# Performance work log

Hardware: AMD Instinct MI355X
Metric: run time of the kernel (lower is better)

Reference implementation:

```python
import jax, jax.numpy as jnp
import numpy as np

THRESHOLD = 1.0  # snntorch Leaky default threshold
BETA = 0.9
ATAN_ALPHA = 2.0  # snntorch surrogate.atan default alpha

# Heaviside forward with ATan surrogate gradient (snntorch surrogate.atan)
@jax.custom_vjp
def atan_spike(x):
    return (x > 0).astype(x.dtype)

def _atan_fwd(x):
    return atan_spike(x), x

def _atan_bwd(x, g):
    # d/dx ~ (alpha/2) / (1 + (pi/2 * alpha * x)^2)
    return (g * (ATAN_ALPHA / 2.0) / (1.0 + (jnp.pi / 2.0 * ATAN_ALPHA * x) ** 2),)

atan_spike.defvjp(_atan_fwd, _atan_bwd)


def setup_inputs() -> dict:
    key = jax.random.key(0)
    kx, kw = jax.random.split(key)
    T, B, N_in, N_out = 128, 64, 1024, 1024
    x = (jax.random.uniform(kx, (T, B, N_in)) < 0.2).astype(jnp.float32)
    # kaiming_uniform_(mode='fan_in', nonlinearity='tanh'): gain=5/3, bound=gain*sqrt(3/fan_in)
    bound = (5.0 / 3.0) * np.sqrt(3.0 / N_in)
    W = jax.random.uniform(kw, (N_out, N_in), minval=-bound, maxval=bound, dtype=jnp.float32)
    return {"x": x, "W": W}


def reference(x, W):
    # x: (T, B, N_in) -> current: (T, B, N_out) via bias-free linear (vmapped over T)
    cur = jnp.einsum('tbi,oi->tbo', x, W)
    mem0 = jnp.zeros(cur.shape[1:], cur.dtype)

    # snntorch Leaky (reset_mechanism='subtract'):
    #   reset_t = detached spike of previous mem; mem_t = beta*mem_{t-1} + I_t - reset_t*thr
    #   spk_t = fire(mem_t)
    def step(mem, c_t):
        reset = jax.lax.stop_gradient(atan_spike(mem - THRESHOLD))
        mem_new = BETA * mem + c_t - reset * THRESHOLD
        spk = atan_spike(mem_new - THRESHOLD)
        return mem_new, (spk, mem_new)

    _, (spk_rec, mem_rec) = jax.lax.scan(step, mem0, cur)
    return spk_rec, mem_rec
```

## Files before the change

kernel.cpp:

```cpp
#include <hip/hip_runtime.h>
#include <cstddef>

constexpr int T_STEPS = 128;
constexpr int BATCH   = 64;
constexpr int N_IN    = 1024;
constexpr int N_OUT   = 1024;
constexpr int M_TOTAL = T_STEPS * BATCH;
constexpr int NEURONS = BATCH * N_OUT;
constexpr int OUT_HALF = T_STEPS * NEURONS;

constexpr double W_SCALE     = 17179869184.0;
constexpr double W_INV_SCALE = 1.0 / 17179869184.0;

typedef int   i32x4 __attribute__((ext_vector_type(4)));
typedef float f32x4 __attribute__((ext_vector_type(4)));

__global__ __launch_bounds__(256)
void prep_all(const float* __restrict__ x, const float* __restrict__ W,
              signed char* __restrict__ xi8, signed char* __restrict__ pi8)
{
    const int bid = blockIdx.x;
    if (bid < 2048) {
        const int i = bid * 256 + threadIdx.x;
        const float4 a = ((const float4*)x)[4 * i + 0];
        const float4 b = ((const float4*)x)[4 * i + 1];
        const float4 c = ((const float4*)x)[4 * i + 2];
        const float4 d = ((const float4*)x)[4 * i + 3];
        const float f[16] = {a.x,a.y,a.z,a.w, b.x,b.y,b.z,b.w,
                             c.x,c.y,c.z,c.w, d.x,d.y,d.z,d.w};
        union { signed char b[16]; int4 v; } u;
#pragma unroll
        for (int j = 0; j < 16; ++j) u.b[j] = (signed char)(f[j] != 0.0f);
        ((int4*)xi8)[i] = u.v;
    } else {
        const int i = (bid - 2048) * 256 + threadIdx.x;
        const float4 wv = ((const float4*)W)[i];
        const float wf[4] = {wv.x, wv.y, wv.z, wv.w};
        union { signed char b[4]; unsigned u; } dig[4];
#pragma unroll
        for (int j = 0; j < 4; ++j) {
            int q = __double2int_rn((double)wf[j] * W_SCALE);
            const int d0 = ((q + 128) & 255) - 128;  q = (q - d0) >> 8;
            const int d1 = ((q + 128) & 255) - 128;  q = (q - d1) >> 8;
            const int d2 = ((q + 128) & 255) - 128;  q = (q - d2) >> 8;
            dig[0].b[j] = (signed char)d0;
            dig[1].b[j] = (signed char)d1;
            dig[2].b[j] = (signed char)d2;
            dig[3].b[j] = (signed char)q;
        }
        unsigned* pw = (unsigned*)pi8;
#pragma unroll
        for (int p = 0; p < 4; ++p) pw[p * 262144 + i] = dig[p].u;
    }
}

constexpr int LDT = 80;

__global__ __launch_bounds__(512)
void gemm_planes(const signed char* __restrict__ xi8, const signed char* __restrict__ pi8,
                 unsigned* __restrict__ outw)
{
    __shared__ __align__(16) signed char As[128][LDT];
    __shared__ __align__(16) signed char Bs[4][128][LDT];

    const int tid  = threadIdx.x;
    const int m0   = blockIdx.x * 128;
    const int n0   = blockIdx.y * 128;
    const int lane = tid & 63;
    const int w    = tid >> 6;
    const int wm   = w >> 2;
    const int wn   = w & 3;
    const int l15  = lane & 15;
    const int kg   = lane >> 4;

    i32x4 acc[4][4][2] = {};

    const int arow = tid >> 2;
    const int aq   = tid & 3;

    for (int k0 = 0; k0 < N_IN; k0 += 64) {
        {
            const int4 v = *(const int4*)(xi8 + (size_t)(m0 + arow) * N_IN + k0 + aq * 16);
            *(int4*)(&As[arow][aq * 16]) = v;
        }
#pragma unroll
        for (int r = 0; r < 4; ++r) {
            const int u2  = tid + 512 * r;
            const int p   = u2 >> 9;
            const int rem = u2 & 511;
            const int row = rem >> 2;
            const int qq  = rem & 3;
            const int4 v = *(const int4*)(pi8 + (size_t)p * 1048576
                                              + (size_t)(n0 + row) * N_IN + k0 + qq * 16);
            *(int4*)(&Bs[p][row][qq * 16]) = v;
        }
        __syncthreads();

        i32x4 af[4], bf[2][4];
#pragma unroll
        for (int fm = 0; fm < 4; ++fm)
            af[fm] = *(const i32x4*)(&As[wm * 64 + fm * 16 + l15][kg * 16]);
#pragma unroll
        for (int fn = 0; fn < 2; ++fn)
#pragma unroll
            for (int p = 0; p < 4; ++p)
                bf[fn][p] = *(const i32x4*)(&Bs[p][wn * 32 + fn * 16 + l15][kg * 16]);

#pragma unroll
        for (int p = 0; p < 4; ++p)
#pragma unroll
            for (int fm = 0; fm < 4; ++fm)
#pragma unroll
                for (int fn = 0; fn < 2; ++fn)
                    acc[p][fm][fn] = __builtin_amdgcn_mfma_i32_16x16x64_i8(
                        af[fm], bf[fn][p], acc[p][fm][fn], 0, 0, 0);
        __syncthreads();
    }

#pragma unroll
    for (int fm = 0; fm < 4; ++fm)
#pragma unroll
        for (int fn = 0; fn < 2; ++fn)
#pragma unroll
            for (int r = 0; r < 4; ++r) {
                const int m = m0 + wm * 64 + fm * 16 + kg * 4 + r;
                const int o = n0 + wn * 32 + fn * 16 + l15;
                const double q = (double)acc[3][fm][fn][r] * 16777216.0
                               + (double)acc[2][fm][fn][r] * 65536.0
                               + (double)acc[1][fm][fn][r] * 256.0
                               + (double)acc[0][fm][fn][r];
                const double cur = q * W_INV_SCALE;
                const unsigned long long u = (unsigned long long)__double_as_longlong(cur);
                const int t = m >> 6;
                const int b = m & 63;
                const size_t idx = (size_t)t * NEURONS + (size_t)b * N_OUT + o;
                outw[idx]            = (unsigned)u;
                outw[OUT_HALF + idx] = (unsigned)(u >> 32);
            }
}

__global__ __launch_bounds__(256)
void lif_scan(unsigned* outw)
{
    const int n = (blockIdx.x * 256 + threadIdx.x) * 2;
    double mem0 = 0.0, mem1 = 0.0;
    double c0[8], c1[8];
    for (int t0 = 0; t0 < T_STEPS; t0 += 8) {
#pragma unroll
        for (int j = 0; j < 8; ++j) {
            const size_t idx = (size_t)(t0 + j) * NEURONS + n;
            const uint2 lo = *(const uint2*)(outw + idx);
            const uint2 hi = *(const uint2*)(outw + OUT_HALF + idx);
            c0[j] = __longlong_as_double((long long)(((unsigned long long)hi.x << 32) | lo.x));
            c1[j] = __longlong_as_double((long long)(((unsigned long long)hi.y << 32) | lo.y));
        }
#pragma unroll
        for (int j = 0; j < 8; ++j) {
            const double r0 = (mem0 > 1.0) ? 1.0 : 0.0;
            const double r1 = (mem1 > 1.0) ? 1.0 : 0.0;
            mem0 = 0.9 * mem0 + c0[j] - r0;
            mem1 = 0.9 * mem1 + c1[j] - r1;
            const size_t idx = (size_t)(t0 + j) * NEURONS + n;
            uint2 s, mv;
            s.x  = (mem0 > 1.0) ? 0x3f800000u : 0u;
            s.y  = (mem1 > 1.0) ? 0x3f800000u : 0u;
            mv.x = __float_as_uint((float)mem0);
            mv.y = __float_as_uint((float)mem1);
            *(uint2*)(outw + idx)            = s;
            *(uint2*)(outw + OUT_HALF + idx) = mv;
        }
    }
}

extern "C" void kernel_launch(void* const* d_in, const int* in_sizes, int n_in,
                              void* d_out, int out_size, void* d_ws, size_t ws_size,
                              hipStream_t stream)
{
    const float* x = (const float*)d_in[0];
    const float* W = (const float*)d_in[1];
    unsigned* outw = (unsigned*)d_out;

    signed char* xi8 = (signed char*)d_ws;
    signed char* pi8 = xi8 + (size_t)M_TOTAL * N_IN;

    prep_all<<<3072, 256, 0, stream>>>(x, W, xi8, pi8);

    dim3 ggrid(M_TOTAL / 128, N_OUT / 128);
    gemm_planes<<<ggrid, 512, 0, stream>>>(xi8, pi8, outw);

    lif_scan<<<NEURONS / 512, 256, 0, stream>>>(outw);
}
```

Baseline: 161.0 us.

## Use direct global-to-LDS loads with XOR swizzle and prefetch in LIF scan

The GEMM tile loads now go through global_load_lds, which writes global data straight into LDS without passing through registers. The padded LDS layout is replaced by an unpadded one with an XOR chunk swizzle to avoid bank conflicts. The LIF scan moves to one neuron per thread with twice as many blocks, and it software-prefetches the next 8 timesteps while computing the current ones. The risks are ordering and correctness subtleties in the async LDS writes (visibility relies on __syncthreads) and a changed memory access pattern in the scan.

New measurement: 161.4 us. No clear change (+0.2%).

```diff
diff --git a/kernel.cpp b/kernel.cpp
--- a/kernel.cpp
+++ b/kernel.cpp
@@ -12,8 +12,7 @@
 constexpr double W_SCALE     = 17179869184.0;
 constexpr double W_INV_SCALE = 1.0 / 17179869184.0;
 
-typedef int   i32x4 __attribute__((ext_vector_type(4)));
-typedef float f32x4 __attribute__((ext_vector_type(4)));
+typedef int i32x4 __attribute__((ext_vector_type(4)));
 
 __global__ __launch_bounds__(256)
 void prep_all(const float* __restrict__ x, const float* __restrict__ W,
@@ -54,14 +53,19 @@
     }
 }
 
-constexpr int LDT = 80;
+__device__ __forceinline__ void gload_lds16(const signed char* g, signed char* l)
+{
+    __builtin_amdgcn_global_load_lds(
+        (const __attribute__((address_space(1))) unsigned*)(g),
+        (__attribute__((address_space(3))) unsigned*)(l), 16, 0, 0);
+}
 
 __global__ __launch_bounds__(512)
 void gemm_planes(const signed char* __restrict__ xi8, const signed char* __restrict__ pi8,
                  unsigned* __restrict__ outw)
 {
-    __shared__ __align__(16) signed char As[128][LDT];
-    __shared__ __align__(16) signed char Bs[4][128][LDT];
+    __shared__ __align__(16) signed char As[128 * 64];
+    __shared__ __align__(16) signed char Bs[4 * 128 * 64];
 
     const int tid  = threadIdx.x;
     const int m0   = blockIdx.x * 128;
@@ -72,39 +76,40 @@
     const int wn   = w & 3;
     const int l15  = lane & 15;
     const int kg   = lane >> 4;
+    const int swzr = (l15 >> 1) & 3;
+
+    const int srow   = lane >> 2;
+    const int schunk = (lane & 3) ^ ((lane >> 3) & 3);
 
     i32x4 acc[4][4][2] = {};
 
-    const int arow = tid >> 2;
-    const int aq   = tid & 3;
-
     for (int k0 = 0; k0 < N_IN; k0 += 64) {
-        {
-            const int4 v = *(const int4*)(xi8 + (size_t)(m0 + arow) * N_IN + k0 + aq * 16);
-            *(int4*)(&As[arow][aq * 16]) = v;
-        }
-#pragma unroll
-        for (int r = 0; r < 4; ++r) {
-            const int u2  = tid + 512 * r;
-            const int p   = u2 >> 9;
-            const int rem = u2 & 511;
-            const int row = rem >> 2;
-            const int qq  = rem & 3;
-            const int4 v = *(const int4*)(pi8 + (size_t)p * 1048576
-                                              + (size_t)(n0 + row) * N_IN + k0 + qq * 16);
-            *(int4*)(&Bs[p][row][qq * 16]) = v;
+        gload_lds16(xi8 + (size_t)(m0 + w * 16 + srow) * N_IN + k0 + schunk * 16,
+                    As + w * 1024);
+#pragma unroll
+        for (int i = 0; i < 4; ++i) {
+            const int seg  = w * 4 + i;
+            const int p    = seg >> 3;
+            const int rowp = (seg & 7) * 16 + srow;
+            gload_lds16(pi8 + (size_t)p * 1048576 + (size_t)(n0 + rowp) * N_IN
+                            + k0 + schunk * 16,
+                        Bs + seg * 1024);
         }
         __syncthreads();
 
         i32x4 af[4], bf[2][4];
 #pragma unroll
-        for (int fm = 0; fm < 4; ++fm)
-            af[fm] = *(const i32x4*)(&As[wm * 64 + fm * 16 + l15][kg * 16]);
-#pragma unroll
-        for (int fn = 0; fn < 2; ++fn)
+        for (int fm = 0; fm < 4; ++fm) {
+            const int row = wm * 64 + fm * 16 + l15;
+            af[fm] = *(const i32x4*)(As + row * 64 + (kg ^ swzr) * 16);
+        }
+#pragma unroll
+        for (int fn = 0; fn < 2; ++fn) {
+            const int row = wn * 32 + fn * 16 + l15;
 #pragma unroll
             for (int p = 0; p < 4; ++p)
-                bf[fn][p] = *(const i32x4*)(&Bs[p][wn * 32 + fn * 16 + l15][kg * 16]);
+                bf[fn][p] = *(const i32x4*)(Bs + p * 8192 + row * 64 + (kg ^ swzr) * 16);
+        }
 
 #pragma unroll
         for (int p = 0; p < 4; ++p)
@@ -142,33 +147,36 @@
 __global__ __launch_bounds__(256)
 void lif_scan(unsigned* outw)
 {
-    const int n = (blockIdx.x * 256 + threadIdx.x) * 2;
-    double mem0 = 0.0, mem1 = 0.0;
-    double c0[8], c1[8];
+    const int n = blockIdx.x * 256 + threadIdx.x;
+    double mem = 0.0;
+    double c[8], cn[8];
+#pragma unroll
+    for (int j = 0; j < 8; ++j) {
+        const size_t idx = (size_t)j * NEURONS + n;
+        const unsigned lo = outw[idx];
+        const unsigned hi = outw[OUT_HALF + idx];
+        c[j] = __longlong_as_double((long long)(((unsigned long long)hi << 32) | lo));
+    }
     for (int t0 = 0; t0 < T_STEPS; t0 += 8) {
+        if (t0 + 8 < T_STEPS) {
+#pragma unroll
+            for (int j = 0; j < 8; ++j) {
+                const size_t idx = (size_t)(t0 + 8 + j) * NEURONS + n;
+                const unsigned lo = outw[idx];
+                const unsigned hi = outw[OUT_HALF + idx];
+                cn[j] = __longlong_as_double((long long)(((unsigned long long)hi << 32) | lo));
+            }
+        }
 #pragma unroll
         for (int j = 0; j < 8; ++j) {
+            const double reset = (mem > 1.0) ? 1.0 : 0.0;
+            mem = 0.9 * mem + c[j] - reset;
             const size_t idx = (size_t)(t0 + j) * NEURONS + n;
-            const uint2 lo = *(const uint2*)(outw + idx);
-            const uint2 hi = *(const uint2*)(outw + OUT_HALF + idx);
-            c0[j] = __longlong_as_double((long long)(((unsigned long long)hi.x << 32) | lo.x));
-            c1[j] = __longlong_as_double((long long)(((unsigned long long)hi.y << 32) | lo.y));
-        }
-#pragma unroll
-        for (int j = 0; j < 8; ++j) {
-            const double r0 = (mem0 > 1.0) ? 1.0 : 0.0;
-            const double r1 = (mem1 > 1.0) ? 1.0 : 0.0;
-            mem0 = 0.9 * mem0 + c0[j] - r0;
-            mem1 = 0.9 * mem1 + c1[j] - r1;
-            const size_t idx = (size_t)(t0 + j) * NEURONS + n;
-            uint2 s, mv;
-            s.x  = (mem0 > 1.0) ? 0x3f800000u : 0u;
-            s.y  = (mem1 > 1.0) ? 0x3f800000u : 0u;
-            mv.x = __float_as_uint((float)mem0);
-            mv.y = __float_as_uint((float)mem1);
-            *(uint2*)(outw + idx)            = s;
-            *(uint2*)(outw + OUT_HALF + idx) = mv;
-        }
+            outw[idx]            = (mem > 1.0) ? 0x3f800000u : 0u;
+            outw[OUT_HALF + idx] = __float_as_uint((float)mem);
+        }
+#pragma unroll
+        for (int j = 0; j < 8; ++j) c[j] = cn[j];
     }
 }
 
@@ -188,5 +196,5 @@
     dim3 ggrid(M_TOTAL / 128, N_OUT / 128);
     gemm_planes<<<ggrid, 512, 0, stream>>>(xi8, pi8, outw);
 
-    lif_scan<<<NEURONS / 512, 256, 0, stream>>>(outw);
-}
+    lif_scan<<<NEURONS / 256, 256, 0, stream>>>(outw);
+}
```
